# Kernel tuning notes

Hardware: AMD Instinct MI355X
Metric: run time of the kernel (lower is better)

## Reference

```python
import jax, jax.numpy as jnp
import numpy as np

B, S, D, H = 2, 2048, 1024, 16  # batch, seq, d_model, num_heads
DH = D // H


def setup_inputs() -> dict:
    key = jax.random.key(0)
    ks = jax.random.split(key, 11)
    sc = 1.0 / np.sqrt(D)
    return {
        "q": jax.random.normal(ks[0], (B, S, D), jnp.float32),
        "k": jax.random.normal(ks[1], (B, S, D), jnp.float32),
        "v": jax.random.normal(ks[2], (B, S, D), jnp.float32),
        "wq": jax.random.normal(ks[3], (D, D), jnp.float32) * sc,
        "bq": jax.random.normal(ks[4], (D,), jnp.float32) * 0.01,
        "wk": jax.random.normal(ks[5], (D, D), jnp.float32) * sc,
        "bk": jax.random.normal(ks[6], (D,), jnp.float32) * 0.01,
        "wv": jax.random.normal(ks[7], (D, D), jnp.float32) * sc,
        "bv": jax.random.normal(ks[8], (D,), jnp.float32) * 0.01,
        "wo": jax.random.normal(ks[9], (D, D), jnp.float32) * sc,
        "bo": jax.random.normal(ks[10], (D,), jnp.float32) * 0.01,
    }


def reference(q, k, v, wq, bq, wk, bk, wv, bv, wo, bo):
    # projections: [B,S,D]
    query = q @ wq + bq
    key_ = k @ wk + bk
    value = v @ wv + bv
    # split heads: [B,H,S,DH]
    def split(x):
        return jnp.transpose(x.reshape(B, S, H, DH), (0, 2, 1, 3))
    query, key_, value = split(query), split(key_), split(value)
    # NOTE: original module applies NO 1/sqrt(d_k) scaling
    scores = jnp.einsum("bhqd,bhkd->bhqk", query, key_)
    attn = jax.nn.softmax(scores, axis=-1)
    data = jnp.einsum("bhqk,bhkd->bhqd", attn, value)  # [B,H,S,DH]
    # faithful to original bug: transpose(0,1) then view(B,S,-1)
    data = jnp.swapaxes(data, 0, 1).reshape(B, S, D)
    return data @ wo + bo
```

## Files before the change

### kernel.cpp

```cpp
#include <hip/hip_runtime.h>

typedef _Float16 f16;
typedef _Float16 f16x8 __attribute__((ext_vector_type(8)));
typedef _Float16 f16x4 __attribute__((ext_vector_type(4)));
typedef float    f32x4 __attribute__((ext_vector_type(4)));

static constexpr int BATCH = 2, SEQ = 2048, DMODEL = 1024, HEADS = 16, DHEAD = 64;
static constexpr int MTOK = BATCH * SEQ;
static constexpr float LOG2E = 1.44269504088896f;

#define GLOBAL_LOAD_LDS16(gptr, lptr)                                              \
  __builtin_amdgcn_global_load_lds(                                                \
      (const __attribute__((address_space(1))) void*)(gptr),                       \
      (__attribute__((address_space(3))) void*)(lptr), 16, 0, 0)

#define MFMA16(a, b, c) __builtin_amdgcn_mfma_f32_16x16x32_f16((a), (b), (c), 0, 0, 0)

__device__ __forceinline__ float fexp2(float x) {
  float r;
  asm volatile("v_exp_f32 %0, %1" : "=v"(r) : "v"(x));
  return r;
}

__device__ __forceinline__ int imgAB(int mr, int kr) {
  int pr = mr >> 1;
  int jj = ((mr & 1) << 2) | (kr >> 3);
  int j = jj ^ (pr & 7);
  return pr * 64 + j * 8 + (kr & 7);
}
__device__ __forceinline__ int imgK(int sr, int dh) {
  return sr * 64 + (((dh >> 3) ^ (sr & 7)) << 3) + (dh & 7);
}

__global__ __launch_bounds__(256) void cast_kernel(const float* __restrict__ src,
                                                   f16* __restrict__ dst) {
  int c = blockIdx.x * 256 + threadIdx.x;
  int blk = c >> 8, cb = c & 255;
  int pr = cb >> 3, j = cb & 7;
  int jj = j ^ (pr & 7);
  int mr = (pr << 1) | (jj >> 2);
  int kr = (jj & 3) << 3;
  int m = (blk >> 5) * 64 + mr;
  int k = (blk & 31) * 32 + kr;
  const float* s = src + (size_t)m * DMODEL + k;
  f32x4 a = *(const f32x4*)s, b = *(const f32x4*)(s + 4);
  f16x8 o;
  o[0] = (f16)a[0]; o[1] = (f16)a[1]; o[2] = (f16)a[2]; o[3] = (f16)a[3];
  o[4] = (f16)b[0]; o[5] = (f16)b[1]; o[6] = (f16)b[2]; o[7] = (f16)b[3];
  *(f16x8*)(dst + (size_t)c * 8) = o;
}

__global__ __launch_bounds__(256) void transw_kernel(
    const float* __restrict__ w0, const float* __restrict__ w1,
    const float* __restrict__ w2, const float* __restrict__ w3,
    f16* __restrict__ Wimg) {
  const int z = blockIdx.z;
  const float* w = z == 0 ? w0 : z == 1 ? w1 : z == 2 ? w2 : w3;
  f16* t = Wimg + (size_t)z * DMODEL * DMODEL;
  __shared__ f16 lt[64][72];
  const int k0 = blockIdx.x * 64, n0 = blockIdx.y * 64;
  const int r = threadIdx.x >> 2, c0 = (threadIdx.x & 3) * 16;
  const float* src = w + (size_t)(k0 + r) * DMODEL + n0 + c0;
#pragma unroll
  for (int jx = 0; jx < 16; jx += 4) {
    f32x4 x = *(const f32x4*)(src + jx);
    lt[c0 + jx + 0][r] = (f16)x[0];
    lt[c0 + jx + 1][r] = (f16)x[1];
    lt[c0 + jx + 2][r] = (f16)x[2];
    lt[c0 + jx + 3][r] = (f16)x[3];
  }
  __syncthreads();
  const int n = n0 + r;
#pragma unroll
  for (int cw = 0; cw < 2; cw++) {
    int k = k0 + c0 + cw * 8;
    int blk = ((n >> 6) << 5) | (k >> 5);
    int off = blk * 2048 + imgAB(n & 63, k & 31);
    f16x8 v;
#pragma unroll
    for (int e = 0; e < 8; e++) v[e] = lt[r][c0 + cw * 8 + e];
    *(f16x8*)(t + off) = v;
  }
}

__global__ __launch_bounds__(256) void proj_kernel(
    const f16* __restrict__ Ximg, const f16* __restrict__ Wimg,
    const float* __restrict__ bq, const float* __restrict__ bk,
    const float* __restrict__ bv, f16* __restrict__ Qp, f16* __restrict__ Kp,
    f16* __restrict__ Vt, int zbase, size_t aStride) {
  __shared__ f16 As[4096];
  __shared__ f16 Bs[4096];
  const int z = zbase + blockIdx.z;
  const f16* A = Ximg + (size_t)blockIdx.z * aStride;
  const f16* Bw = Wimg + (size_t)z * DMODEL * DMODEL;
  int lin = blockIdx.x + (blockIdx.y << 3);
  int swz = ((lin & 7) << 5) + (lin >> 3);
  const int n0 = (swz & 7) * 128, m0 = (swz >> 3) * 128;
  const int tid = threadIdx.x, w = tid >> 6, l = tid & 63, q = l & 15, g = l >> 4;
  const int wr = w >> 1, wc = w & 1;
  const int KT = DMODEL >> 5;
  int aoff[4], boff[4];
#pragma unroll
  for (int mi = 0; mi < 4; mi++) {
    int mr = wr * 64 + mi * 16 + q;
    aoff[mi] = ((mr >> 6) << 11) + imgAB(mr & 63, g * 8);
  }
#pragma unroll
  for (int ni = 0; ni < 4; ni++) {
    int nr = wc * 64 + ni * 16 + q;
    boff[ni] = ((nr >> 6) << 11) + imgAB(nr & 63, g * 8);
  }
  f32x4 acc[4][4] = {};
  for (int t = 0; t < KT; t++) {
#pragma unroll
    for (int i = 0; i < 2; i++) {
      int c = w * 2 + i;
      GLOBAL_LOAD_LDS16(A + (size_t)(((m0 >> 6) + (c >> 2)) * KT + t) * 2048 + (c & 3) * 512 + l * 8,
                        (char*)&As[c * 512]);
      GLOBAL_LOAD_LDS16(Bw + (size_t)(((n0 >> 6) + (c >> 2)) * KT + t) * 2048 + (c & 3) * 512 + l * 8,
                        (char*)&Bs[c * 512]);
    }
    __syncthreads();
    f16x8 af[4], bf[4];
#pragma unroll
    for (int mi = 0; mi < 4; mi++) af[mi] = *(const f16x8*)&As[aoff[mi]];
#pragma unroll
    for (int ni = 0; ni < 4; ni++) bf[ni] = *(const f16x8*)&Bs[boff[ni]];
#pragma unroll
    for (int mi = 0; mi < 4; mi++)
#pragma unroll
      for (int ni = 0; ni < 4; ni++)
        acc[mi][ni] = MFMA16(af[mi], bf[ni], acc[mi][ni]);
    __syncthreads();
  }
  const float* bias = z == 0 ? bq : (z == 1 ? bk : bv);
#pragma unroll
  for (int mi = 0; mi < 4; mi++)
#pragma unroll
    for (int ni = 0; ni < 4; ni++) {
      const int col = n0 + wc * 64 + ni * 16 + q;
      const float bvl = bias[col];
      const int row0 = m0 + wr * 64 + mi * 16 + g * 4;
      if (z == 0) {
#pragma unroll
        for (int r = 0; r < 4; r++)
          Qp[(size_t)(row0 + r) * DMODEL + col] = (f16)((acc[mi][ni][r] + bvl) * LOG2E);
      } else if (z == 1) {
        const int h = col >> 6, dh = col & 63;
#pragma unroll
        for (int r = 0; r < 4; r++) {
          const int row = row0 + r, s = row & (SEQ - 1);
          Kp[(size_t)(((row >> 11) * HEADS + h) * 64 + (s >> 5)) * 2048 + imgK(s & 31, dh)] =
              (f16)(acc[mi][ni][r] + bvl);
        }
      } else {
        const int h = col >> 6, dh = col & 63;
        const int s0 = row0 & (SEQ - 1);
        f16* dst = Vt + (size_t)(((row0 >> 11) * HEADS + h) * 64 + (s0 >> 5)) * 2048 +
                   imgAB(dh, s0 & 31);
        f16x4 ov;
        ov[0] = (f16)(acc[mi][ni][0] + bvl); ov[1] = (f16)(acc[mi][ni][1] + bvl);
        ov[2] = (f16)(acc[mi][ni][2] + bvl); ov[3] = (f16)(acc[mi][ni][3] + bvl);
        *(f16x4*)dst = ov;
      }
    }
}

__global__ __launch_bounds__(256) void attn_kernel(
    const f16* __restrict__ Qp, const f16* __restrict__ Kimg,
    const f16* __restrict__ Vimg, f16* __restrict__ Simg) {
  __shared__ f16 Klds[2][2048];
  __shared__ f16 Vlds[2][2048];
  __shared__ f16 Plds[4][512];
  const int tid = threadIdx.x, w = tid >> 6, l = tid & 63, q = l & 15, g = l >> 4;
  int lin = blockIdx.x + (blockIdx.y << 5);
  int swz = ((lin & 7) << 7) + (lin >> 3);
  const int qb = swz & 31, bh = swz >> 5;
  const int b = bh >> 4, h = bh & 15;
  const int q0 = qb * 64 + w * 16;
  const f16* qrow = Qp + (size_t)(b * SEQ + q0 + q) * DMODEL + h * 64;
  const f16x8 qf0 = *(const f16x8*)(qrow + g * 8);
  const f16x8 qf1 = *(const f16x8*)(qrow + 32 + g * 8);
  const f16* kt_base = Kimg + (size_t)(bh * 64) * 2048;
  const f16* vt_base = Vimg + (size_t)(bh * 64) * 2048;
  int koff[2][2];
#pragma unroll
  for (int fn = 0; fn < 2; fn++)
#pragma unroll
    for (int hf = 0; hf < 2; hf++) koff[fn][hf] = imgK(fn * 16 + q, hf * 32 + g * 8);
  int voff[4];
#pragma unroll
  for (int fo = 0; fo < 4; fo++) voff[fo] = imgAB(fo * 16 + q, g * 8);
  const int poff = imgAB(q, g * 8);
  int pwoff[2];
  {
    const int pr = q >> 1;
#pragma unroll
    for (int fn = 0; fn < 2; fn++) {
      int jj = ((q & 1) << 2) | (fn * 2 + (g >> 1));
      pwoff[fn] = pr * 64 + ((jj ^ (pr & 7)) << 3) + (g & 1) * 4;
    }
  }
  f16* Pw = &Plds[w][0];
  float m_st = -1.0e30f, l_pt = 0.f;
  f32x4 o_acc[4] = {};

  GLOBAL_LOAD_LDS16(kt_base + w * 512 + l * 8, (char*)&Klds[0][w * 512]);
  GLOBAL_LOAD_LDS16(vt_base + w * 512 + l * 8, (char*)&Vlds[0][w * 512]);
  __syncthreads();

  for (int t = 0; t < 64; t++) {
    const int bb = t & 1;
    if (t < 63) {
      GLOBAL_LOAD_LDS16(kt_base + (size_t)(t + 1) * 2048 + w * 512 + l * 8,
                        (char*)&Klds[bb ^ 1][w * 512]);
      GLOBAL_LOAD_LDS16(vt_base + (size_t)(t + 1) * 2048 + w * 512 + l * 8,
                        (char*)&Vlds[bb ^ 1][w * 512]);
    }
    const f16* Kb = &Klds[bb][0];
    const f16* Vb = &Vlds[bb][0];
    f32x4 s0 = {}, s1 = {};
    s0 = MFMA16(*(const f16x8*)(Kb + koff[0][0]), qf0, s0);
    s0 = MFMA16(*(const f16x8*)(Kb + koff[0][1]), qf1, s0);
    s1 = MFMA16(*(const f16x8*)(Kb + koff[1][0]), qf0, s1);
    s1 = MFMA16(*(const f16x8*)(Kb + koff[1][1]), qf1, s1);
    float lm = fmaxf(fmaxf(fmaxf(s0[0], s0[1]), fmaxf(s0[2], s0[3])),
                     fmaxf(fmaxf(s1[0], s1[1]), fmaxf(s1[2], s1[3])));
    if (!__all(lm <= m_st + 8.f)) {
      float mx = lm;
      mx = fmaxf(mx, __shfl_xor(mx, 16, 64));
      mx = fmaxf(mx, __shfl_xor(mx, 32, 64));
      const float mnew = fmaxf(m_st, mx);
      const float sc = fexp2(m_st - mnew);
      m_st = mnew;
      l_pt *= sc;
#pragma unroll
      for (int fo = 0; fo < 4; fo++) {
        o_acc[fo][0] *= sc; o_acc[fo][1] *= sc;
        o_acc[fo][2] *= sc; o_acc[fo][3] *= sc;
      }
    }
    f16x4 pa, pb;
    float ts = 0.f;
#pragma unroll
    for (int r = 0; r < 4; r++) {
      float e0 = fexp2(s0[r] - m_st);
      float e1 = fexp2(s1[r] - m_st);
      ts += e0 + e1;
      pa[r] = (f16)e0;
      pb[r] = (f16)e1;
    }
    l_pt += ts;
    *(f16x4*)(Pw + pwoff[0]) = pa;
    *(f16x4*)(Pw + pwoff[1]) = pb;
    const f16x8 pf = *(const f16x8*)(Pw + poff);
#pragma unroll
    for (int fo = 0; fo < 4; fo++)
      o_acc[fo] = MFMA16(*(const f16x8*)(Vb + voff[fo]), pf, o_acc[fo]);
    __syncthreads();
  }
  float lsum = l_pt + __shfl_xor(l_pt, 16, 64);
  lsum += __shfl_xor(lsum, 32, 64);
  const float inv = 1.f / lsum;
  const int s = q0 + q;
  const int m16 = (2 * h + b) & 15, bp = h >> 3;
  const int tp = bp * SEQ + m16 * 128 + (s >> 4);
#pragma unroll
  for (int fo = 0; fo < 4; fo++) {
    const int d0 = (s & 15) * 64 + fo * 16 + g * 4;
    f16* dst = Simg + (size_t)(((tp >> 6) << 5) | (d0 >> 5)) * 2048 + imgAB(tp & 63, d0 & 31);
    f16x4 ov;
    ov[0] = (f16)(o_acc[fo][0] * inv); ov[1] = (f16)(o_acc[fo][1] * inv);
    ov[2] = (f16)(o_acc[fo][2] * inv); ov[3] = (f16)(o_acc[fo][3] * inv);
    *(f16x4*)dst = ov;
  }
}

__global__ __launch_bounds__(256) void ogemm_kernel(
    const f16* __restrict__ Aimg, const f16* __restrict__ Bimg,
    const float* __restrict__ bias, float* __restrict__ out) {
  __shared__ f16 As[4096];
  __shared__ f16 Bs[2048];
  int lin = blockIdx.x + (blockIdx.y << 4);
  int swz = ((lin & 7) << 6) + (lin >> 3);
  const int n0 = (swz & 15) * 64, m0 = (swz >> 4) * 128;
  const int tid = threadIdx.x, w = tid >> 6, l = tid & 63, q = l & 15, g = l >> 4;
  const int wr = w >> 1, wc = w & 1;
  int aoff[4], boff[2];
#pragma unroll
  for (int mi = 0; mi < 4; mi++) {
    int mr = wr * 64 + mi * 16 + q;
    aoff[mi] = ((mr >> 6) << 11) + imgAB(mr & 63, g * 8);
  }
#pragma unroll
  for (int ni = 0; ni < 2; ni++) boff[ni] = imgAB(wc * 32 + ni * 16 + q, g * 8);
  f32x4 acc[4][2] = {};
  for (int t = 0; t < 32; t++) {
#pragma unroll
    for (int i = 0; i < 2; i++) {
      int c = w * 2 + i;
      GLOBAL_LOAD_LDS16(Aimg + (size_t)(((m0 >> 6) + (c >> 2)) * 32 + t) * 2048 + (c & 3) * 512 + l * 8,
                        (char*)&As[c * 512]);
    }
    GLOBAL_LOAD_LDS16(Bimg + ((size_t)(n0 >> 6) * 32 + t) * 2048 + w * 512 + l * 8,
                      (char*)&Bs[w * 512]);
    __syncthreads();
    f16x8 af[4], bf[2];
#pragma unroll
    for (int mi = 0; mi < 4; mi++) af[mi] = *(const f16x8*)&As[aoff[mi]];
#pragma unroll
    for (int ni = 0; ni < 2; ni++) bf[ni] = *(const f16x8*)&Bs[boff[ni]];
#pragma unroll
    for (int mi = 0; mi < 4; mi++)
#pragma unroll
      for (int ni = 0; ni < 2; ni++)
        acc[mi][ni] = MFMA16(af[mi], bf[ni], acc[mi][ni]);
    __syncthreads();
  }
#pragma unroll
  for (int mi = 0; mi < 4; mi++)
#pragma unroll
    for (int ni = 0; ni < 2; ni++) {
      const int col = n0 + wc * 32 + ni * 16 + q;
      const float bvl = bias[col];
      const int row0 = m0 + wr * 64 + mi * 16 + g * 4;
#pragma unroll
      for (int r = 0; r < 4; r++)
        out[(size_t)(row0 + r) * DMODEL + col] = acc[mi][ni][r] + bvl;
    }
}

extern "C" void kernel_launch(void* const* d_in, const int* in_sizes, int n_in,
                              void* d_out, int out_size, void* d_ws, size_t ws_size,
                              hipStream_t stream) {
  const float* q  = (const float*)d_in[0];
  const float* k  = (const float*)d_in[1];
  const float* v  = (const float*)d_in[2];
  const float* wq = (const float*)d_in[3];
  const float* bq = (const float*)d_in[4];
  const float* wk = (const float*)d_in[5];
  const float* bk = (const float*)d_in[6];
  const float* wv = (const float*)d_in[7];
  const float* bv = (const float*)d_in[8];
  const float* wo = (const float*)d_in[9];
  const float* bo = (const float*)d_in[10];

  const size_t XSZ = (size_t)MTOK * DMODEL;
  f16* ws = (f16*)d_ws;
  const bool fused = ws_size >= (56ull << 20);

  f16 *X0, *X1, *X2, *Qp, *Kp, *Vt, *Wimg, *scr;
  if (fused) {
    X0 = ws; X1 = ws + XSZ; X2 = ws + 2 * XSZ;
    Qp = ws + 3 * XSZ; Kp = ws + 4 * XSZ; Vt = ws + 5 * XSZ;
    Wimg = ws + 6 * XSZ;
    scr = X0;
  } else {
    X0 = X1 = X2 = ws;
    Qp = ws + XSZ; Kp = ws + 2 * XSZ; Vt = ws + 3 * XSZ;
    Wimg = ws + 4 * XSZ;
    scr = X0;
  }

  dim3 blk(256);
  dim3 gT(16, 16, 4);
  dim3 gC(2048);
  dim3 gA(32, 32);
  dim3 gO(16, 32);

  transw_kernel<<<gT, blk, 0, stream>>>(wq, wk, wv, wo, Wimg);

  if (fused) {
    cast_kernel<<<gC, blk, 0, stream>>>(q, X0);
    cast_kernel<<<gC, blk, 0, stream>>>(k, X1);
    cast_kernel<<<gC, blk, 0, stream>>>(v, X2);
    proj_kernel<<<dim3(8, 32, 3), blk, 0, stream>>>(X0, Wimg, bq, bk, bv, Qp, Kp, Vt, 0, XSZ);
  } else {
    cast_kernel<<<gC, blk, 0, stream>>>(q, X0);
    proj_kernel<<<dim3(8, 32, 1), blk, 0, stream>>>(X0, Wimg, bq, bk, bv, Qp, Kp, Vt, 0, 0);
    cast_kernel<<<gC, blk, 0, stream>>>(k, X0);
    proj_kernel<<<dim3(8, 32, 1), blk, 0, stream>>>(X0, Wimg, bq, bk, bv, Qp, Kp, Vt, 1, 0);
    cast_kernel<<<gC, blk, 0, stream>>>(v, X0);
    proj_kernel<<<dim3(8, 32, 1), blk, 0, stream>>>(X0, Wimg, bq, bk, bv, Qp, Kp, Vt, 2, 0);
  }

  attn_kernel<<<gA, blk, 0, stream>>>(Qp, Kp, Vt, scr);
  ogemm_kernel<<<gO, blk, 0, stream>>>(scr, Wimg + (size_t)3 * DMODEL * DMODEL, bo, (float*)d_out);
}
```

Before: 247.2 us.

## Double-buffer LDS loads in GEMMs and widen attention KV tiles

Proj and output GEMM kernels now use double-buffered LDS with prefetch of the next K-tile, explicit vmcnt waits and raw s_barrier in place of __syncthreads. The attention kernel processes 64 keys per iteration (two 32-key sub-tiles), splits K and V loading across waves, double-buffers P in LDS, and uses a 1D grid with a launch bound of 4 blocks. The aim is to overlap global-to-LDS transfer with MFMA work and halve the barrier count in attention, at the cost of more LDS per block and possible occupancy loss. Relying on vmcnt alone may leave LDS visibility races if the direct-to-LDS loads need further waits.

Result: no change. 244.0 us (-1.3%).

```diff
diff --git a/kernel.cpp b/kernel.cpp
--- a/kernel.cpp
+++ b/kernel.cpp
@@ -15,6 +15,9 @@
       (__attribute__((address_space(3))) void*)(lptr), 16, 0, 0)
 
 #define MFMA16(a, b, c) __builtin_amdgcn_mfma_f32_16x16x32_f16((a), (b), (c), 0, 0, 0)
+
+#define WAITV_(N) asm volatile("s_waitcnt vmcnt(" #N ")" ::: "memory")
+#define WAITV(N) WAITV_(N)
 
 __device__ __forceinline__ float fexp2(float x) {
   float r;
@@ -88,8 +91,8 @@
     const float* __restrict__ bq, const float* __restrict__ bk,
     const float* __restrict__ bv, f16* __restrict__ Qp, f16* __restrict__ Kp,
     f16* __restrict__ Vt, int zbase, size_t aStride) {
-  __shared__ f16 As[4096];
-  __shared__ f16 Bs[4096];
+  __shared__ f16 As[2][4096];
+  __shared__ f16 Bs[2][4096];
   const int z = zbase + blockIdx.z;
   const f16* A = Ximg + (size_t)blockIdx.z * aStride;
   const f16* Bw = Wimg + (size_t)z * DMODEL * DMODEL;
@@ -111,27 +114,42 @@
     boff[ni] = ((nr >> 6) << 11) + imgAB(nr & 63, g * 8);
   }
   f32x4 acc[4][4] = {};
+
+#define PROJ_STAGE(bb, t)                                                          \
+  {                                                                                \
+    _Pragma("unroll")                                                              \
+    for (int i = 0; i < 2; i++) {                                                  \
+      int c = w * 2 + i;                                                           \
+      size_t ga = (size_t)(((m0 >> 6) + (c >> 2)) * KT + (t)) * 2048 +             \
+                  (c & 3) * 512 + l * 8;                                           \
+      GLOBAL_LOAD_LDS16(A + ga, (char*)&As[bb][c * 512]);                          \
+      size_t gb = (size_t)(((n0 >> 6) + (c >> 2)) * KT + (t)) * 2048 +             \
+                  (c & 3) * 512 + l * 8;                                           \
+      GLOBAL_LOAD_LDS16(Bw + gb, (char*)&Bs[bb][c * 512]);                         \
+    }                                                                              \
+  }
+
+  PROJ_STAGE(0, 0);
   for (int t = 0; t < KT; t++) {
-#pragma unroll
-    for (int i = 0; i < 2; i++) {
-      int c = w * 2 + i;
-      GLOBAL_LOAD_LDS16(A + (size_t)(((m0 >> 6) + (c >> 2)) * KT + t) * 2048 + (c & 3) * 512 + l * 8,
-                        (char*)&As[c * 512]);
-      GLOBAL_LOAD_LDS16(Bw + (size_t)(((n0 >> 6) + (c >> 2)) * KT + t) * 2048 + (c & 3) * 512 + l * 8,
-                        (char*)&Bs[c * 512]);
-    }
-    __syncthreads();
+    const int bb = t & 1;
+    if (t < KT - 1) {
+      PROJ_STAGE(bb ^ 1, t + 1);
+      WAITV(4);
+    } else {
+      WAITV(0);
+    }
+    __builtin_amdgcn_s_barrier();
     f16x8 af[4], bf[4];
 #pragma unroll
-    for (int mi = 0; mi < 4; mi++) af[mi] = *(const f16x8*)&As[aoff[mi]];
-#pragma unroll
-    for (int ni = 0; ni < 4; ni++) bf[ni] = *(const f16x8*)&Bs[boff[ni]];
+    for (int mi = 0; mi < 4; mi++) af[mi] = *(const f16x8*)&As[bb][aoff[mi]];
+#pragma unroll
+    for (int ni = 0; ni < 4; ni++) bf[ni] = *(const f16x8*)&Bs[bb][boff[ni]];
 #pragma unroll
     for (int mi = 0; mi < 4; mi++)
 #pragma unroll
       for (int ni = 0; ni < 4; ni++)
         acc[mi][ni] = MFMA16(af[mi], bf[ni], acc[mi][ni]);
-    __syncthreads();
+    __builtin_amdgcn_s_barrier();
   }
   const float* bias = z == 0 ? bq : (z == 1 ? bk : bv);
 #pragma unroll
@@ -166,28 +184,31 @@
     }
 }
 
-__global__ __launch_bounds__(256) void attn_kernel(
+__global__ __launch_bounds__(256, 4) void attn_kernel(
     const f16* __restrict__ Qp, const f16* __restrict__ Kimg,
     const f16* __restrict__ Vimg, f16* __restrict__ Simg) {
-  __shared__ f16 Klds[2][2048];
-  __shared__ f16 Vlds[2][2048];
-  __shared__ f16 Plds[4][512];
+  __shared__ f16 Klds[2][2][2048];
+  __shared__ f16 Vlds[2][2][2048];
+  __shared__ f16 Plds[4][2][512];
   const int tid = threadIdx.x, w = tid >> 6, l = tid & 63, q = l & 15, g = l >> 4;
-  int lin = blockIdx.x + (blockIdx.y << 5);
-  int swz = ((lin & 7) << 7) + (lin >> 3);
+  const int lin = blockIdx.x;
+  const int swz = ((lin & 7) << 7) + (lin >> 3);
   const int qb = swz & 31, bh = swz >> 5;
   const int b = bh >> 4, h = bh & 15;
   const int q0 = qb * 64 + w * 16;
+
   const f16* qrow = Qp + (size_t)(b * SEQ + q0 + q) * DMODEL + h * 64;
   const f16x8 qf0 = *(const f16x8*)(qrow + g * 8);
   const f16x8 qf1 = *(const f16x8*)(qrow + 32 + g * 8);
   const f16* kt_base = Kimg + (size_t)(bh * 64) * 2048;
   const f16* vt_base = Vimg + (size_t)(bh * 64) * 2048;
-  int koff[2][2];
-#pragma unroll
-  for (int fn = 0; fn < 2; fn++)
-#pragma unroll
-    for (int hf = 0; hf < 2; hf++) koff[fn][hf] = imgK(fn * 16 + q, hf * 32 + g * 8);
+
+  int koff[4][2];
+#pragma unroll
+  for (int fn = 0; fn < 4; fn++)
+#pragma unroll
+    for (int hf = 0; hf < 2; hf++)
+      koff[fn][hf] = (fn >> 1) * 2048 + imgK((fn & 1) * 16 + q, hf * 32 + g * 8);
   int voff[4];
 #pragma unroll
   for (int fo = 0; fo < 4; fo++) voff[fo] = imgAB(fo * 16 + q, g * 8);
@@ -201,34 +222,45 @@
       pwoff[fn] = pr * 64 + ((jj ^ (pr & 7)) << 3) + (g & 1) * 4;
     }
   }
-  f16* Pw = &Plds[w][0];
   float m_st = -1.0e30f, l_pt = 0.f;
   f32x4 o_acc[4] = {};
 
-  GLOBAL_LOAD_LDS16(kt_base + w * 512 + l * 8, (char*)&Klds[0][w * 512]);
-  GLOBAL_LOAD_LDS16(vt_base + w * 512 + l * 8, (char*)&Vlds[0][w * 512]);
-  __syncthreads();
-
-  for (int t = 0; t < 64; t++) {
+#define ATTN_STAGE(bb, t)                                                          \
+  {                                                                                \
+    const f16* sb_ = (w < 2) ? (kt_base + (size_t)(2 * (t) + w) * 2048)            \
+                             : (vt_base + (size_t)(2 * (t) + (w - 2)) * 2048);     \
+    f16* db_ = (w < 2) ? &Klds[bb][w][0] : &Vlds[bb][w - 2][0];                    \
+    _Pragma("unroll")                                                              \
+    for (int j_ = 0; j_ < 4; j_++)                                                 \
+      GLOBAL_LOAD_LDS16(sb_ + j_ * 512 + l * 8, (char*)(db_ + j_ * 512));          \
+  }
+
+  ATTN_STAGE(0, 0);
+  for (int t = 0; t < 32; t++) {
     const int bb = t & 1;
-    if (t < 63) {
-      GLOBAL_LOAD_LDS16(kt_base + (size_t)(t + 1) * 2048 + w * 512 + l * 8,
-                        (char*)&Klds[bb ^ 1][w * 512]);
-      GLOBAL_LOAD_LDS16(vt_base + (size_t)(t + 1) * 2048 + w * 512 + l * 8,
-                        (char*)&Vlds[bb ^ 1][w * 512]);
-    }
-    const f16* Kb = &Klds[bb][0];
-    const f16* Vb = &Vlds[bb][0];
-    f32x4 s0 = {}, s1 = {};
-    s0 = MFMA16(*(const f16x8*)(Kb + koff[0][0]), qf0, s0);
-    s0 = MFMA16(*(const f16x8*)(Kb + koff[0][1]), qf1, s0);
-    s1 = MFMA16(*(const f16x8*)(Kb + koff[1][0]), qf0, s1);
-    s1 = MFMA16(*(const f16x8*)(Kb + koff[1][1]), qf1, s1);
-    float lm = fmaxf(fmaxf(fmaxf(s0[0], s0[1]), fmaxf(s0[2], s0[3])),
-                     fmaxf(fmaxf(s1[0], s1[1]), fmaxf(s1[2], s1[3])));
+    if (t < 31) {
+      ATTN_STAGE(bb ^ 1, t + 1);
+      WAITV(4);
+    } else {
+      WAITV(0);
+    }
+    __builtin_amdgcn_s_barrier();
+    const f16* Kb = &Klds[bb][0][0];
+    f32x4 sacc[4];
+#pragma unroll
+    for (int fn = 0; fn < 4; fn++) {
+      f32x4 zz = {};
+      zz = MFMA16(*(const f16x8*)(Kb + koff[fn][0]), qf0, zz);
+      zz = MFMA16(*(const f16x8*)(Kb + koff[fn][1]), qf1, zz);
+      sacc[fn] = zz;
+    }
+    float lm = fmaxf(
+        fmaxf(fmaxf(fmaxf(sacc[0][0], sacc[0][1]), fmaxf(sacc[0][2], sacc[0][3])),
+              fmaxf(fmaxf(sacc[1][0], sacc[1][1]), fmaxf(sacc[1][2], sacc[1][3]))),
+        fmaxf(fmaxf(fmaxf(sacc[2][0], sacc[2][1]), fmaxf(sacc[2][2], sacc[2][3])),
+              fmaxf(fmaxf(sacc[3][0], sacc[3][1]), fmaxf(sacc[3][2], sacc[3][3]))));
     if (!__all(lm <= m_st + 8.f)) {
-      float mx = lm;
-      mx = fmaxf(mx, __shfl_xor(mx, 16, 64));
+      float mx = fmaxf(lm, __shfl_xor(lm, 16, 64));
       mx = fmaxf(mx, __shfl_xor(mx, 32, 64));
       const float mnew = fmaxf(m_st, mx);
       const float sc = fexp2(m_st - mnew);
@@ -240,24 +272,28 @@
         o_acc[fo][2] *= sc; o_acc[fo][3] *= sc;
       }
     }
-    f16x4 pa, pb;
     float ts = 0.f;
 #pragma unroll
-    for (int r = 0; r < 4; r++) {
-      float e0 = fexp2(s0[r] - m_st);
-      float e1 = fexp2(s1[r] - m_st);
-      ts += e0 + e1;
-      pa[r] = (f16)e0;
-      pb[r] = (f16)e1;
+    for (int fn = 0; fn < 4; fn++) {
+      f16x4 pk;
+#pragma unroll
+      for (int r = 0; r < 4; r++) {
+        float e = fexp2(sacc[fn][r] - m_st);
+        ts += e;
+        pk[r] = (f16)e;
+      }
+      *(f16x4*)(&Plds[w][fn >> 1][0] + pwoff[fn & 1]) = pk;
     }
     l_pt += ts;
-    *(f16x4*)(Pw + pwoff[0]) = pa;
-    *(f16x4*)(Pw + pwoff[1]) = pb;
-    const f16x8 pf = *(const f16x8*)(Pw + poff);
-#pragma unroll
-    for (int fo = 0; fo < 4; fo++)
-      o_acc[fo] = MFMA16(*(const f16x8*)(Vb + voff[fo]), pf, o_acc[fo]);
-    __syncthreads();
+    const f16x8 p0 = *(const f16x8*)(&Plds[w][0][0] + poff);
+    const f16x8 p1 = *(const f16x8*)(&Plds[w][1][0] + poff);
+    const f16* Vb = &Vlds[bb][0][0];
+#pragma unroll
+    for (int fo = 0; fo < 4; fo++) {
+      o_acc[fo] = MFMA16(*(const f16x8*)(Vb + voff[fo]), p0, o_acc[fo]);
+      o_acc[fo] = MFMA16(*(const f16x8*)(Vb + 2048 + voff[fo]), p1, o_acc[fo]);
+    }
+    __builtin_amdgcn_s_barrier();
   }
   float lsum = l_pt + __shfl_xor(l_pt, 16, 64);
   lsum += __shfl_xor(lsum, 32, 64);
@@ -279,8 +315,8 @@
 __global__ __launch_bounds__(256) void ogemm_kernel(
     const f16* __restrict__ Aimg, const f16* __restrict__ Bimg,
     const float* __restrict__ bias, float* __restrict__ out) {
-  __shared__ f16 As[4096];
-  __shared__ f16 Bs[2048];
+  __shared__ f16 As[2][4096];
+  __shared__ f16 Bs[2][2048];
   int lin = blockIdx.x + (blockIdx.y << 4);
   int swz = ((lin & 7) << 6) + (lin >> 3);
   const int n0 = (swz & 15) * 64, m0 = (swz >> 4) * 128;
@@ -295,27 +331,41 @@
 #pragma unroll
   for (int ni = 0; ni < 2; ni++) boff[ni] = imgAB(wc * 32 + ni * 16 + q, g * 8);
   f32x4 acc[4][2] = {};
+
+#define OG_STAGE(bb, t)                                                            \
+  {                                                                                \
+    _Pragma("unroll")                                                              \
+    for (int i = 0; i < 2; i++) {                                                  \
+      int c = w * 2 + i;                                                           \
+      size_t ga = (size_t)(((m0 >> 6) + (c >> 2)) * 32 + (t)) * 2048 +             \
+                  (c & 3) * 512 + l * 8;                                           \
+      GLOBAL_LOAD_LDS16(Aimg + ga, (char*)&As[bb][c * 512]);                       \
+    }                                                                              \
+    size_t gb = (size_t)((n0 >> 6) * 32 + (t)) * 2048 + w * 512 + l * 8;           \
+    GLOBAL_LOAD_LDS16(Bimg + gb, (char*)&Bs[bb][w * 512]);                         \
+  }
+
+  OG_STAGE(0, 0);
   for (int t = 0; t < 32; t++) {
-#pragma unroll
-    for (int i = 0; i < 2; i++) {
-      int c = w * 2 + i;
-      GLOBAL_LOAD_LDS16(Aimg + (size_t)(((m0 >> 6) + (c >> 2)) * 32 + t) * 2048 + (c & 3) * 512 + l * 8,
-                        (char*)&As[c * 512]);
-    }
-    GLOBAL_LOAD_LDS16(Bimg + ((size_t)(n0 >> 6) * 32 + t) * 2048 + w * 512 + l * 8,
-                      (char*)&Bs[w * 512]);
-    __syncthreads();
+    const int bb = t & 1;
+    if (t < 31) {
+      OG_STAGE(bb ^ 1, t + 1);
+      WAITV(3);
+    } else {
+      WAITV(0);
+    }
+    __builtin_amdgcn_s_barrier();
     f16x8 af[4], bf[2];
 #pragma unroll
-    for (int mi = 0; mi < 4; mi++) af[mi] = *(const f16x8*)&As[aoff[mi]];
-#pragma unroll
-    for (int ni = 0; ni < 2; ni++) bf[ni] = *(const f16x8*)&Bs[boff[ni]];
+    for (int mi = 0; mi < 4; mi++) af[mi] = *(const f16x8*)&As[bb][aoff[mi]];
+#pragma unroll
+    for (int ni = 0; ni < 2; ni++) bf[ni] = *(const f16x8*)&Bs[bb][boff[ni]];
 #pragma unroll
     for (int mi = 0; mi < 4; mi++)
 #pragma unroll
       for (int ni = 0; ni < 2; ni++)
         acc[mi][ni] = MFMA16(af[mi], bf[ni], acc[mi][ni]);
-    __syncthreads();
+    __builtin_amdgcn_s_barrier();
   }
 #pragma unroll
   for (int mi = 0; mi < 4; mi++)
@@ -365,7 +415,7 @@
   dim3 blk(256);
   dim3 gT(16, 16, 4);
   dim3 gC(2048);
-  dim3 gA(32, 32);
+  dim3 gA(1024);
   dim3 gO(16, 32);
 
   transw_kernel<<<gT, blk, 0, stream>>>(wq, wk, wv, wo, Wimg);
```
